# Optimization experiments

Hardware: AMD Instinct MI355X
Metric: run time of the kernel (lower is better)

The kernel has to match this reference:

```python
import jax, jax.numpy as jnp
import numpy as np

KERNEL_SIZE = 15
PAD = (KERNEL_SIZE - 1) // 2


def _dark_channel(x):
    # x: [B, 3, H, W] in [-1, 1]
    x = (x + 1.0) / 2.0
    x = jnp.min(x, axis=1, keepdims=True)            # channel min -> [B,1,H,W]
    x = jnp.pad(x, ((0, 0), (0, 0), (PAD, PAD), (PAD, PAD)), mode='reflect')
    # sliding-window min (morphological erosion), VALID after reflect pad
    x = jax.lax.reduce_window(
        x, jnp.inf, jax.lax.min,
        window_dimensions=(1, 1, KERNEL_SIZE, KERNEL_SIZE),
        window_strides=(1, 1, 1, 1),
        padding='VALID')
    return jnp.clip(x, 0.0, 0.1)


def setup_inputs() -> dict:
    key = jax.random.key(0)
    k1, k2 = jax.random.split(key)
    shape = (16, 3, 512, 512)
    # tanh-range images in [-1, 1]
    real = jax.random.uniform(k1, shape, dtype=jnp.float32) * 2.0 - 1.0
    fake = jax.random.uniform(k2, shape, dtype=jnp.float32) * 2.0 - 1.0
    return {"real": real, "fake": fake}


def reference(real, fake):
    real_map = _dark_channel(real)
    fake_map = _dark_channel(fake)
    diff = real_map - fake_map
    return jnp.mean(diff * diff)  # nn.MSELoss (mean reduction)
```

## Files before the change

### kernel.cpp

```cpp
#include <hip/hip_runtime.h>

#define BDIM 256
#define TILE 64
#define HALO 7
#define IN_T 78
#define CSTR 84
#define VSTR 82
#define IMG 512
#define HW (IMG * IMG)
#define NPIX (16.0f * 512.0f * 512.0f)
#define P1_TASKS (IN_T * 20)
#define P1_ITERS 7
#define NBLOCKS 1024

typedef float f4 __attribute__((ext_vector_type(4)));

__device__ __forceinline__ int reflect_idx(int i, int n) {
    i = (i < 0) ? -i : i;
    i = (i >= n) ? (2 * n - 2 - i) : i;
    return i;
}

__device__ __forceinline__ unsigned short umin16(unsigned short a, unsigned short b) {
    return a < b ? a : b;
}

__device__ __forceinline__ unsigned short map_bf16(float v) {
    float m = fminf(fmaxf(fmaf(v, 0.5f, 0.5f), 0.0f), 0.1f);
    unsigned int u = __float_as_uint(m);
    return (unsigned short)((u + 0x7fffu + ((u >> 16) & 1u)) >> 16);
}

__device__ __forceinline__ float bf16_f32(unsigned short x) {
    return __uint_as_float(((unsigned int)x) << 16);
}

__device__ __forceinline__ void dark_tile(const float* __restrict__ X,
                                          unsigned short* __restrict__ cmin,
                                          unsigned short* __restrict__ vm,
                                          int tid, int r0g, int c0g, bool fastcol,
                                          float (&o)[16]) {
    #pragma unroll
    for (int i = 0; i < P1_ITERS; ++i) {
        int t = tid + i * BDIM;
        t = t < (P1_TASKS - 1) ? t : (P1_TASKS - 1);
        int row = (unsigned)t / 20u;
        int g = t - row * 20;
        int gr = reflect_idx(r0g + row, IMG);
        const float* rp = X + (size_t)gr * IMG;
        unsigned short w[4];
        if (fastcol) {
            const float* p = rp + (c0g - 1 + 4 * g);
            f4 a = *(const f4*)p;
            f4 b = *(const f4*)(p + HW);
            f4 c = *(const f4*)(p + 2 * HW);
            #pragma unroll
            for (int k = 0; k < 4; ++k)
                w[k] = map_bf16(fminf(a[k], fminf(b[k], c[k])));
        } else {
            #pragma unroll
            for (int k = 0; k < 4; ++k) {
                int gc = reflect_idx(c0g - 1 + 4 * g + k, IMG);
                float v = fminf(rp[gc], fminf(rp[HW + gc], rp[2 * HW + gc]));
                w[k] = map_bf16(v);
            }
        }
        uint2 pk;
        pk.x = (unsigned)w[0] | ((unsigned)w[1] << 16);
        pk.y = (unsigned)w[2] | ((unsigned)w[3] << 16);
        *(uint2*)&cmin[row * CSTR + 4 * g] = pk;
    }
    __syncthreads();

    #pragma unroll
    for (int b = 0; b < 2; ++b) {
        int t = tid + b * BDIM;
        if (t < IN_T * 4) {
            int col = (unsigned)t % (unsigned)IN_T;
            int rr0 = ((unsigned)t / (unsigned)IN_T) * 16;
            const unsigned short* cp = cmin + (col + 1);
            unsigned short s[15];
            #pragma unroll
            for (int j = 0; j < 15; ++j) s[j] = cp[(rr0 + j) * CSTR];
            #pragma unroll
            for (int j = 13; j >= 0; --j) s[j] = umin16(s[j], s[j + 1]);
            unsigned short* vp = vm + col;
            vp[rr0 * VSTR] = s[0];
            unsigned short f = cp[(rr0 + 15) * CSTR];
            #pragma unroll
            for (int i2 = 1; i2 <= 14; ++i2) {
                vp[(rr0 + i2) * VSTR] = umin16(s[i2], f);
                f = umin16(f, cp[(rr0 + 15 + i2) * CSTR]);
            }
            vp[(rr0 + 15) * VSTR] = f;
        }
    }
    __syncthreads();

    {
        int row = tid >> 2, k = tid & 3;
        const unsigned int* vr = (const unsigned int*)(vm + row * VSTR) + 8 * k;
        unsigned short x[32];
        #pragma unroll
        for (int j = 0; j < 16; ++j) {
            unsigned int d = vr[j];
            x[2 * j] = (unsigned short)d;
            x[2 * j + 1] = (unsigned short)(d >> 16);
        }
        unsigned short s[15];
        #pragma unroll
        for (int j = 0; j < 15; ++j) s[j] = x[j];
        #pragma unroll
        for (int j = 13; j >= 0; --j) s[j] = umin16(s[j], s[j + 1]);
        o[0] = bf16_f32(s[0]);
        unsigned short f = x[15];
        #pragma unroll
        for (int i2 = 1; i2 <= 14; ++i2) {
            o[i2] = bf16_f32(umin16(s[i2], f));
            f = umin16(f, x[15 + i2]);
        }
        o[15] = bf16_f32(f);
    }
}

__global__ __launch_bounds__(BDIM, 4)
void dcl_kernel(const float* __restrict__ real, const float* __restrict__ fake,
                float* __restrict__ ws) {
    __shared__ __align__(8) unsigned short cmin[IN_T * CSTR];
    __shared__ __align__(8) unsigned short vm[TILE * VSTR];
    __shared__ float red[BDIM / 64];

    const int tid = threadIdx.x;
    const int r0g = blockIdx.y * TILE - HALO;
    const int c0g = blockIdx.x * TILE - HALO;
    const bool fastcol = (c0g >= 1) && (c0g + 79 <= IMG);
    const size_t ib = (size_t)blockIdx.z * 3 * HW;

    float o_r[16], o_f[16];
    dark_tile(real + ib, cmin, vm, tid, r0g, c0g, fastcol, o_r);
    dark_tile(fake + ib, cmin, vm, tid, r0g, c0g, fastcol, o_f);

    float acc = 0.f;
    #pragma unroll
    for (int i = 0; i < 16; ++i) {
        float d = o_r[i] - o_f[i];
        acc += d * d;
    }
    #pragma unroll
    for (int off = 32; off >= 1; off >>= 1)
        acc += __shfl_xor(acc, off, 64);
    if ((tid & 63) == 0) red[tid >> 6] = acc;
    __syncthreads();
    if (tid == 0) {
        int bid = blockIdx.x + 8 * (blockIdx.y + 8 * blockIdx.z);
        ws[bid] = red[0] + red[1] + red[2] + red[3];
    }
}

__global__ __launch_bounds__(256)
void reduce_kernel(const float* __restrict__ ws, float* __restrict__ out) {
    __shared__ float red[4];
    int tid = threadIdx.x;
    float a = ws[tid] + ws[tid + 256] + ws[tid + 512] + ws[tid + 768];
    #pragma unroll
    for (int off = 32; off >= 1; off >>= 1)
        a += __shfl_xor(a, off, 64);
    if ((tid & 63) == 0) red[tid >> 6] = a;
    __syncthreads();
    if (tid == 0)
        out[0] = (red[0] + red[1] + red[2] + red[3]) * (1.0f / NPIX);
}

extern "C" void kernel_launch(void* const* d_in, const int* in_sizes, int n_in,
                              void* d_out, int out_size, void* d_ws, size_t ws_size,
                              hipStream_t stream) {
    const float* real = (const float*)d_in[0];
    const float* fake = (const float*)d_in[1];
    float* ws = (float*)d_ws;
    float* out = (float*)d_out;
    dim3 grid(IMG / TILE, IMG / TILE, 16);
    dcl_kernel<<<grid, BDIM, 0, stream>>>(real, fake, ws);
    reduce_kernel<<<1, 256, 0, stream>>>(ws, out);
}
```

Measured before the change: 140.1 us.

## Load real and fake tiles together with double-buffered loads and XCD-aware block mapping

```diff
diff --git a/kernel.cpp b/kernel.cpp
--- a/kernel.cpp
+++ b/kernel.cpp
@@ -10,8 +10,7 @@
 #define HW (IMG * IMG)
 #define NPIX (16.0f * 512.0f * 512.0f)
 #define P1_TASKS (IN_T * 20)
-#define P1_ITERS 7
-#define NBLOCKS 1024
+#define NBLK 1024
 
 typedef float f4 __attribute__((ext_vector_type(4)));
 
@@ -35,50 +34,15 @@
     return __uint_as_float(((unsigned int)x) << 16);
 }
 
-__device__ __forceinline__ void dark_tile(const float* __restrict__ X,
-                                          unsigned short* __restrict__ cmin,
-                                          unsigned short* __restrict__ vm,
-                                          int tid, int r0g, int c0g, bool fastcol,
-                                          float (&o)[16]) {
-    #pragma unroll
-    for (int i = 0; i < P1_ITERS; ++i) {
-        int t = tid + i * BDIM;
-        t = t < (P1_TASKS - 1) ? t : (P1_TASKS - 1);
-        int row = (unsigned)t / 20u;
-        int g = t - row * 20;
-        int gr = reflect_idx(r0g + row, IMG);
-        const float* rp = X + (size_t)gr * IMG;
-        unsigned short w[4];
-        if (fastcol) {
-            const float* p = rp + (c0g - 1 + 4 * g);
-            f4 a = *(const f4*)p;
-            f4 b = *(const f4*)(p + HW);
-            f4 c = *(const f4*)(p + 2 * HW);
-            #pragma unroll
-            for (int k = 0; k < 4; ++k)
-                w[k] = map_bf16(fminf(a[k], fminf(b[k], c[k])));
-        } else {
-            #pragma unroll
-            for (int k = 0; k < 4; ++k) {
-                int gc = reflect_idx(c0g - 1 + 4 * g + k, IMG);
-                float v = fminf(rp[gc], fminf(rp[HW + gc], rp[2 * HW + gc]));
-                w[k] = map_bf16(v);
-            }
-        }
-        uint2 pk;
-        pk.x = (unsigned)w[0] | ((unsigned)w[1] << 16);
-        pk.y = (unsigned)w[2] | ((unsigned)w[3] << 16);
-        *(uint2*)&cmin[row * CSTR + 4 * g] = pk;
-    }
-    __syncthreads();
-
+__device__ __forceinline__ void phase2(const unsigned short* __restrict__ cm,
+                                       unsigned short* __restrict__ vm, int tid) {
     #pragma unroll
     for (int b = 0; b < 2; ++b) {
         int t = tid + b * BDIM;
         if (t < IN_T * 4) {
             int col = (unsigned)t % (unsigned)IN_T;
             int rr0 = ((unsigned)t / (unsigned)IN_T) * 16;
-            const unsigned short* cp = cmin + (col + 1);
+            const unsigned short* cp = cm + (col + 1);
             unsigned short s[15];
             #pragma unroll
             for (int j = 0; j < 15; ++j) s[j] = cp[(rr0 + j) * CSTR];
@@ -95,50 +59,123 @@
             vp[(rr0 + 15) * VSTR] = f;
         }
     }
-    __syncthreads();
-
-    {
-        int row = tid >> 2, k = tid & 3;
-        const unsigned int* vr = (const unsigned int*)(vm + row * VSTR) + 8 * k;
-        unsigned short x[32];
-        #pragma unroll
-        for (int j = 0; j < 16; ++j) {
-            unsigned int d = vr[j];
-            x[2 * j] = (unsigned short)d;
-            x[2 * j + 1] = (unsigned short)(d >> 16);
-        }
-        unsigned short s[15];
-        #pragma unroll
-        for (int j = 0; j < 15; ++j) s[j] = x[j];
-        #pragma unroll
-        for (int j = 13; j >= 0; --j) s[j] = umin16(s[j], s[j + 1]);
-        o[0] = bf16_f32(s[0]);
-        unsigned short f = x[15];
-        #pragma unroll
-        for (int i2 = 1; i2 <= 14; ++i2) {
-            o[i2] = bf16_f32(umin16(s[i2], f));
-            f = umin16(f, x[15 + i2]);
-        }
-        o[15] = bf16_f32(f);
-    }
+}
+
+__device__ __forceinline__ void phase3(const unsigned short* __restrict__ vm,
+                                       int tid, float (&o)[16]) {
+    int row = tid >> 2, k = tid & 3;
+    const unsigned int* vr = (const unsigned int*)(vm + row * VSTR) + 8 * k;
+    unsigned short x[32];
+    #pragma unroll
+    for (int j = 0; j < 16; ++j) {
+        unsigned int d = vr[j];
+        x[2 * j] = (unsigned short)d;
+        x[2 * j + 1] = (unsigned short)(d >> 16);
+    }
+    unsigned short s[15];
+    #pragma unroll
+    for (int j = 0; j < 15; ++j) s[j] = x[j];
+    #pragma unroll
+    for (int j = 13; j >= 0; --j) s[j] = umin16(s[j], s[j + 1]);
+    o[0] = bf16_f32(s[0]);
+    unsigned short f = x[15];
+    #pragma unroll
+    for (int i2 = 1; i2 <= 14; ++i2) {
+        o[i2] = bf16_f32(umin16(s[i2], f));
+        f = umin16(f, x[15 + i2]);
+    }
+    o[15] = bf16_f32(f);
 }
 
 __global__ __launch_bounds__(BDIM, 4)
 void dcl_kernel(const float* __restrict__ real, const float* __restrict__ fake,
                 float* __restrict__ ws) {
-    __shared__ __align__(8) unsigned short cmin[IN_T * CSTR];
+    __shared__ __align__(8) unsigned short cmr[IN_T * CSTR];
+    __shared__ __align__(8) unsigned short cmf[IN_T * CSTR];
     __shared__ __align__(8) unsigned short vm[TILE * VSTR];
     __shared__ float red[BDIM / 64];
 
     const int tid = threadIdx.x;
-    const int r0g = blockIdx.y * TILE - HALO;
-    const int c0g = blockIdx.x * TILE - HALO;
-    const bool fastcol = (c0g >= 1) && (c0g + 79 <= IMG);
-    const size_t ib = (size_t)blockIdx.z * 3 * HW;
+    const int bid = blockIdx.x;
+    const int xcd = bid & 7;
+    const int s_ = bid >> 3;
+    const int z  = s_ & 15;
+    const int tt = s_ >> 4;
+    const int bx = (xcd & 1) * 4 + (tt & 3);
+    const int by = (xcd >> 1) * 2 + (tt >> 2);
+
+    const int r0g = by * TILE - HALO;
+    const int c0g = bx * TILE - HALO;
+    const bool fastcol = (bx >= 1) && (bx <= 6);
+    const size_t ib = (size_t)z * 3 * HW;
+    const float* __restrict__ Rb = real + ib;
+    const float* __restrict__ Fb = fake + ib;
+
+    f4 bR[2][3], bF[2][3];
+
+    auto load_i = [&](int i, f4 (&R3)[3], f4 (&F3)[3]) {
+        int t = tid + i * BDIM;
+        t = t < (P1_TASKS - 1) ? t : (P1_TASKS - 1);
+        int row = (unsigned)t / 20u;
+        int g = t - row * 20;
+        int gr = reflect_idx(r0g + row, IMG);
+        const float* rpR = Rb + (size_t)gr * IMG;
+        const float* rpF = Fb + (size_t)gr * IMG;
+        if (fastcol) {
+            const float* pR = rpR + (c0g - 1 + 4 * g);
+            const float* pF = rpF + (c0g - 1 + 4 * g);
+            R3[0] = *(const f4*)pR;
+            R3[1] = *(const f4*)(pR + HW);
+            R3[2] = *(const f4*)(pR + 2 * HW);
+            F3[0] = *(const f4*)pF;
+            F3[1] = *(const f4*)(pF + HW);
+            F3[2] = *(const f4*)(pF + 2 * HW);
+        } else {
+            #pragma unroll
+            for (int k = 0; k < 4; ++k) {
+                int gc = reflect_idx(c0g - 1 + 4 * g + k, IMG);
+                R3[0][k] = rpR[gc]; R3[1][k] = rpR[HW + gc]; R3[2][k] = rpR[2 * HW + gc];
+                F3[0][k] = rpF[gc]; F3[1][k] = rpF[HW + gc]; F3[2][k] = rpF[2 * HW + gc];
+            }
+        }
+    };
+
+    auto consume_i = [&](int i, const f4 (&R3)[3], const f4 (&F3)[3]) {
+        int t = tid + i * BDIM;
+        t = t < (P1_TASKS - 1) ? t : (P1_TASKS - 1);
+        int row = (unsigned)t / 20u;
+        int g = t - row * 20;
+        unsigned short wr[4], wf[4];
+        #pragma unroll
+        for (int k = 0; k < 4; ++k) {
+            wr[k] = map_bf16(fminf(R3[0][k], fminf(R3[1][k], R3[2][k])));
+            wf[k] = map_bf16(fminf(F3[0][k], fminf(F3[1][k], F3[2][k])));
+        }
+        uint2 pr, pf;
+        pr.x = (unsigned)wr[0] | ((unsigned)wr[1] << 16);
+        pr.y = (unsigned)wr[2] | ((unsigned)wr[3] << 16);
+        pf.x = (unsigned)wf[0] | ((unsigned)wf[1] << 16);
+        pf.y = (unsigned)wf[2] | ((unsigned)wf[3] << 16);
+        *(uint2*)&cmr[row * CSTR + 4 * g] = pr;
+        *(uint2*)&cmf[row * CSTR + 4 * g] = pf;
+    };
+
+    load_i(0, bR[0], bF[0]);
+    #pragma unroll
+    for (int i = 0; i < 7; ++i) {
+        if (i < 6) load_i(i + 1, bR[(i + 1) & 1], bF[(i + 1) & 1]);
+        consume_i(i, bR[i & 1], bF[i & 1]);
+    }
+    __syncthreads();
 
     float o_r[16], o_f[16];
-    dark_tile(real + ib, cmin, vm, tid, r0g, c0g, fastcol, o_r);
-    dark_tile(fake + ib, cmin, vm, tid, r0g, c0g, fastcol, o_f);
+    phase2(cmr, vm, tid);
+    __syncthreads();
+    phase3(vm, tid, o_r);
+    __syncthreads();
+    phase2(cmf, vm, tid);
+    __syncthreads();
+    phase3(vm, tid, o_f);
 
     float acc = 0.f;
     #pragma unroll
@@ -151,10 +188,8 @@
         acc += __shfl_xor(acc, off, 64);
     if ((tid & 63) == 0) red[tid >> 6] = acc;
     __syncthreads();
-    if (tid == 0) {
-        int bid = blockIdx.x + 8 * (blockIdx.y + 8 * blockIdx.z);
+    if (tid == 0)
         ws[bid] = red[0] + red[1] + red[2] + red[3];
-    }
 }
 
 __global__ __launch_bounds__(256)
@@ -178,7 +213,6 @@
     const float* fake = (const float*)d_in[1];
     float* ws = (float*)d_ws;
     float* out = (float*)d_out;
-    dim3 grid(IMG / TILE, IMG / TILE, 16);
-    dcl_kernel<<<grid, BDIM, 0, stream>>>(real, fake, ws);
+    dcl_kernel<<<dim3(NBLK), BDIM, 0, stream>>>(real, fake, ws);
     reduce_kernel<<<1, 256, 0, stream>>>(ws, out);
 }
```

Result: faster. 132.8 us (-5.2%).
